# Kernel optimization log

Measured on AMD Instinct MI355X. Metric: run time of the kernel, lower is better.

Reference implementation:

```python
import jax, jax.numpy as jnp
import numpy as np

B, T, I, H, O = 256, 512, 64, 512, 1


def _lstm_layer(x, Wih, Whh, bih, bhh):
    # x: [B, T, in]; Wih: [4H, in]; Whh: [4H, H]
    # Precompute input contribution for all timesteps (big GEMM, no recurrence).
    xg = jnp.einsum('bti,gi->btg', x, Wih) + bih + bhh  # [B, T, 4H]
    h0 = jnp.zeros((x.shape[0], Whh.shape[1]), x.dtype)
    c0 = jnp.zeros_like(h0)

    def step(carry, xt):
        h, c = carry
        gates = xt + h @ Whh.T  # [B, 4H]
        i, f, g, o = jnp.split(gates, 4, axis=-1)  # PyTorch gate order i,f,g,o
        i = jax.nn.sigmoid(i)
        f = jax.nn.sigmoid(f)
        g = jnp.tanh(g)
        o = jax.nn.sigmoid(o)
        c = f * c + i * g
        h = o * jnp.tanh(c)
        return (h, c), h

    _, hs = jax.lax.scan(step, (h0, c0), jnp.swapaxes(xg, 0, 1))  # [T, B, H]
    return jnp.swapaxes(hs, 0, 1)  # [B, T, H]


def setup_inputs() -> dict:
    key = jax.random.key(0)
    ks = jax.random.split(key, 12)
    s = 1.0 / np.sqrt(H)
    u = lambda k, shp: jax.random.uniform(k, shp, jnp.float32, -s, s)
    return {
        'x': jax.random.normal(ks[0], (B, T, I), jnp.float32),
        'Wih0': u(ks[1], (4 * H, I)),
        'Whh0': u(ks[2], (4 * H, H)),
        'bih0': u(ks[3], (4 * H,)),
        'bhh0': u(ks[4], (4 * H,)),
        'Wih1': u(ks[5], (4 * H, H)),
        'Whh1': u(ks[6], (4 * H, H)),
        'bih1': u(ks[7], (4 * H,)),
        'bhh1': u(ks[8], (4 * H,)),
        'Wfc': u(ks[9], (O, H)),
        'bfc': u(ks[10], (O,)),
    }


def reference(x, Wih0, Whh0, bih0, bhh0, Wih1, Whh1, bih1, bhh1, Wfc, bfc):
    h1 = _lstm_layer(x, Wih0, Whh0, bih0, bhh0)   # [B, T, H]
    h2 = _lstm_layer(h1, Wih1, Whh1, bih1, bhh1)  # [B, T, H]
    return h2[:, -1] @ Wfc.T + bfc  # [B, O]
```

## Files before the change

kernel.cpp:

```cpp
#include <hip/hip_runtime.h>

typedef unsigned short u16;
typedef unsigned long long u64;
typedef short bf16x8 __attribute__((ext_vector_type(8)));
typedef float f32x4 __attribute__((ext_vector_type(4)));

#define B_ 256
#define T_ 512
#define I_ 64
#define H_ 512
#define RING 32

#define OFF_F0    0u
#define OFF_F1    32768u
#define OFF_F2    65536u
#define OFF_F3    98304u
#define OFF_B0    131072u
#define OFF_B1    139264u
#define OFF_WIH0  147456u
#define OFF_WHH0  409600u
#define OFF_WIH1  2506752u
#define OFF_WHH1  4603904u
#define OFF_HX0   6701056u
#define OFF_HX1   7225344u
#define OFF_H1R   7749632u
#define WS_NEEDED 16138240u

#define AQ __ATOMIC_RELAXED
#define SC __HIP_MEMORY_SCOPE_AGENT

static __device__ __forceinline__ u16 f2b(float f) {
  union { float f; unsigned u; } v; v.f = f;
  unsigned r = (v.u + 0x7FFFu + ((v.u >> 16) & 1u)) >> 16;
  return (u16)r;
}
static __device__ __forceinline__ float sigm(float x) { return 1.f / (1.f + __expf(-x)); }
static __device__ __forceinline__ float tanh_(float x) { return 1.f - 2.f / (__expf(2.f * x) + 1.f); }

__global__ void prep_kernel(const float* __restrict__ Wih0, const float* __restrict__ Whh0,
                            const float* __restrict__ bih0, const float* __restrict__ bhh0,
                            const float* __restrict__ Wih1, const float* __restrict__ Whh1,
                            const float* __restrict__ bih1, const float* __restrict__ bhh1,
                            const float* __restrict__ bfc, float* __restrict__ out,
                            char* __restrict__ ws) {
  unsigned* flags = (unsigned*)(ws + OFF_F0);
  float* b0 = (float*)(ws + OFF_B0);
  float* b1 = (float*)(ws + OFF_B1);
  u16* wih0b = (u16*)(ws + OFF_WIH0);
  u16* whh0b = (u16*)(ws + OFF_WHH0);
  u16* wih1b = (u16*)(ws + OFF_WIH1);
  u16* whh1b = (u16*)(ws + OFF_WHH1);

  long long i = (long long)blockIdx.x * 256 + threadIdx.x;
  if (i < 32768) { __hip_atomic_store(&flags[i], 0u, AQ, SC); return; }
  i -= 32768;
  if (i < 256) { out[i] = bfc[0]; return; }
  i -= 256;
  if (i < 2048) { b0[i] = bih0[i] + bhh0[i]; return; }
  i -= 2048;
  if (i < 2048) { b1[i] = bih1[i] + bhh1[i]; return; }
  i -= 2048;
  if (i < 131072) { wih0b[i] = f2b(Wih0[i]); return; }
  i -= 131072;
  if (i < 1048576) { whh0b[i] = f2b(Whh0[i]); return; }
  i -= 1048576;
  if (i < 1048576) { wih1b[i] = f2b(Wih1[i]); return; }
  i -= 1048576;
  if (i < 1048576) { whh1b[i] = f2b(Whh1[i]); return; }
}

template <bool IS_L0>
__device__ __forceinline__ void lstm_body(
    int bx,
    const float* __restrict__ x,
    const u16* __restrict__ Wib,
    const u16* __restrict__ Whb,
    const float* __restrict__ bias,
    unsigned* __restrict__ hx32,
    u16* __restrict__ h1ring,
    const float* __restrict__ Wfc, float* __restrict__ out,
    unsigned* __restrict__ fR,
    unsigned* __restrict__ fP,
    unsigned* __restrict__ fC,
    float* __restrict__ Gp_s, u16* __restrict__ Ax_s)
{
  const int tid = threadIdx.x;
  const int wv = tid >> 6;
  const int lane = tid & 63;
  const int quad = lane >> 4;
  const int l15 = lane & 15;
  const int jn = bx & 31;
  const int ib = bx >> 5;

  bf16x8 Bh[4][4];
#pragma unroll
  for (int r = 0; r < 4; ++r)
#pragma unroll
    for (int nt = 0; nt < 4; ++nt)
      Bh[r][nt] = *(const bf16x8*)&Whb[(size_t)(nt * 512 + jn * 16 + l15) * 512 +
                                       (wv * 4 + r) * 32 + quad * 8];
  bf16x8 Bx[4][4];
  bf16x8 Bx0[4];
  if constexpr (IS_L0) {
    if (wv < 2) {
#pragma unroll
      for (int nt = 0; nt < 4; ++nt)
        Bx0[nt] = *(const bf16x8*)&Wib[(size_t)(nt * 512 + jn * 16 + l15) * 64 +
                                       wv * 32 + quad * 8];
    }
  } else {
#pragma unroll
    for (int r = 0; r < 4; ++r)
#pragma unroll
      for (int nt = 0; nt < 4; ++nt)
        Bx[r][nt] = *(const bf16x8*)&Wib[(size_t)(nt * 512 + jn * 16 + l15) * 512 +
                                         (wv * 4 + r) * 32 + quad * 8];
  }

  const int erow = tid >> 3;
  const int ecp = tid & 7;
  float bias2[4][2];
#pragma unroll
  for (int g = 0; g < 4; ++g) {
    bias2[g][0] = bias[g * 512 + jn * 16 + 2 * ecp];
    bias2[g][1] = bias[g * 512 + jn * 16 + 2 * ecp + 1];
  }
  float cst2[2] = {0.f, 0.f};
  const f32x4 zf = {0.f, 0.f, 0.f, 0.f};
  const unsigned lineoff = ((unsigned)ib * 32 + jn) * 32;

  const int bg = ib * 32 + erow;
  const int hg = jn * 16 + 2 * ecp;
  const unsigned stoff = (unsigned)(((hg >> 3) * 256 + bg) * 4 + (ecp & 3));

  for (int t = 0; t < T_; ++t) {
    if constexpr (IS_L0) {
      int row = tid >> 3, cc = (tid & 7) * 8;
      const float* xp = x + ((size_t)(ib * 32 + row) * T_ + t) * 64 + cc;
      float4 a = *(const float4*)xp;
      float4 b = *(const float4*)(xp + 4);
      uint4 v;
      v.x = (unsigned)f2b(a.x) | ((unsigned)f2b(a.y) << 16);
      v.y = (unsigned)f2b(a.z) | ((unsigned)f2b(a.w) << 16);
      v.z = (unsigned)f2b(b.x) | ((unsigned)f2b(b.y) << 16);
      v.w = (unsigned)f2b(b.z) | ((unsigned)f2b(b.w) << 16);
      *(uint4*)&Ax_s[row * 72 + cc] = v;
      __syncthreads();
    }

    f32x4 acc[2][4];
#pragma unroll
    for (int mt = 0; mt < 2; ++mt)
#pragma unroll
      for (int nt = 0; nt < 4; ++nt) acc[mt][nt] = zf;

    if constexpr (IS_L0) {
      if (wv < 2) {
        int kk = wv * 32 + quad * 8;
        bf16x8 a0 = *(const bf16x8*)&Ax_s[l15 * 72 + kk];
        bf16x8 a1 = *(const bf16x8*)&Ax_s[(16 + l15) * 72 + kk];
#pragma unroll
        for (int nt = 0; nt < 4; ++nt) {
          acc[0][nt] = __builtin_amdgcn_mfma_f32_16x16x32_bf16(a0, Bx0[nt], acc[0][nt], 0, 0, 0);
          acc[1][nt] = __builtin_amdgcn_mfma_f32_16x16x32_bf16(a1, Bx0[nt], acc[1][nt], 0, 0, 0);
        }
      }
      if (t && wv == 0) {
        unsigned tgtR = (unsigned)t;
        unsigned tgtC = (t >= RING) ? (unsigned)(t - RING + 1) : 0u;
        for (;;) {
          unsigned vv, tg;
          if (lane < 32) { vv = __hip_atomic_load(&fR[lineoff + lane], AQ, SC); tg = tgtR; }
          else           { vv = __hip_atomic_load(&fC[lineoff + lane - 32], AQ, SC); tg = tgtC; }
          if (!__any(vv < tg)) break;
        }
      }
      __syncthreads();
    } else {
      if (wv == 0) {
        unsigned tgtP = (unsigned)(t + 1);
        unsigned tgtR = (unsigned)t;
        for (;;) {
          unsigned vv, tg;
          if (lane < 32) { vv = __hip_atomic_load(&fP[lineoff + lane], AQ, SC); tg = tgtP; }
          else           { vv = __hip_atomic_load(&fR[lineoff + lane - 32], AQ, SC); tg = tgtR; }
          if (!__any(vv < tg)) break;
        }
      }
      __syncthreads();
      const u64* hq1 = (const u64*)h1ring + (size_t)(t & (RING - 1)) * (B_ * H_ / 4);
#pragma unroll
      for (int r = 0; r < 4; ++r) {
        int ks = wv * 4 + r;
        bf16x8 af[2];
#pragma unroll
        for (int mt = 0; mt < 2; ++mt) {
          const u64* p = hq1 + (size_t)((ks * 4 + quad) * 256 + ib * 32 + mt * 16 + l15) * 2;
          union { u64 q[2]; bf16x8 v; } u;
          u.q[0] = __hip_atomic_load(p, AQ, SC);
          u.q[1] = __hip_atomic_load(p + 1, AQ, SC);
          af[mt] = u.v;
        }
#pragma unroll
        for (int nt = 0; nt < 4; ++nt) {
          acc[0][nt] = __builtin_amdgcn_mfma_f32_16x16x32_bf16(af[0], Bx[r][nt], acc[0][nt], 0, 0, 0);
          acc[1][nt] = __builtin_amdgcn_mfma_f32_16x16x32_bf16(af[1], Bx[r][nt], acc[1][nt], 0, 0, 0);
        }
      }
    }

    if (t) {
      const u64* hq = (const u64*)hx32 + (size_t)(t & 1) * (B_ * H_ / 4);
      bf16x8 af[4][2];
#pragma unroll
      for (int r = 0; r < 4; ++r) {
        int ks = wv * 4 + r;
#pragma unroll
        for (int mt = 0; mt < 2; ++mt) {
          const u64* p = hq + (size_t)((ks * 4 + quad) * 256 + ib * 32 + mt * 16 + l15) * 2;
          union { u64 q[2]; bf16x8 v; } u;
          u.q[0] = __hip_atomic_load(p, AQ, SC);
          u.q[1] = __hip_atomic_load(p + 1, AQ, SC);
          af[r][mt] = u.v;
        }
      }
#pragma unroll
      for (int r = 0; r < 4; ++r)
#pragma unroll
        for (int mt = 0; mt < 2; ++mt)
#pragma unroll
          for (int nt = 0; nt < 4; ++nt)
            acc[mt][nt] = __builtin_amdgcn_mfma_f32_16x16x32_bf16(af[r][mt], Bh[r][nt],
                                                                  acc[mt][nt], 0, 0, 0);
    }

#pragma unroll
    for (int mt = 0; mt < 2; ++mt)
#pragma unroll
      for (int nt = 0; nt < 4; ++nt)
#pragma unroll
        for (int rr = 0; rr < 4; ++rr)
          Gp_s[(wv * 32 + mt * 16 + quad * 4 + rr) * 68 + nt * 16 + l15] = acc[mt][nt][rr];
    __syncthreads();

    {
      float pre[4][2];
#pragma unroll
      for (int g = 0; g < 4; ++g) {
        int c = g * 16 + 2 * ecp;
        float s0 = bias2[g][0], s1 = bias2[g][1];
#pragma unroll
        for (int w = 0; w < 4; ++w) {
          s0 += Gp_s[(w * 32 + erow) * 68 + c];
          s1 += Gp_s[(w * 32 + erow) * 68 + c + 1];
        }
        pre[g][0] = s0; pre[g][1] = s1;
      }
      float hv[2];
#pragma unroll
      for (int j = 0; j < 2; ++j) {
        float iv = sigm(pre[0][j]);
        float fv = sigm(pre[1][j]);
        float gv = tanh_(pre[2][j]);
        float ov = sigm(pre[3][j]);
        float cn = fv * cst2[j] + iv * gv;
        cst2[j] = cn;
        hv[j] = ov * tanh_(cn);
      }
      unsigned pack = (unsigned)f2b(hv[0]) | ((unsigned)f2b(hv[1]) << 16);
      __hip_atomic_store(&hx32[(size_t)((t + 1) & 1) * (B_ * H_ / 2) + stoff], pack, AQ, SC);
      if constexpr (IS_L0) {
        unsigned* ring32 = (unsigned*)h1ring;
        __hip_atomic_store(&ring32[(size_t)(t & (RING - 1)) * (B_ * H_ / 2) + stoff],
                           pack, AQ, SC);
      } else if (t == T_ - 1) {
        float part = hv[0] * Wfc[hg] + hv[1] * Wfc[hg + 1];
        part += __shfl_down(part, 4, 8);
        part += __shfl_down(part, 2, 8);
        part += __shfl_down(part, 1, 8);
        if (ecp == 0) atomicAdd(&out[bg], part);
      }
    }

    if constexpr (IS_L0) {
      __syncthreads();
      if (wv == 0) {
        unsigned val = (unsigned)(t + 1);
        if (lane < 32) {
          if (t + 1 < T_)
            __hip_atomic_store(&fR[((unsigned)ib * 32 + lane) * 32 + jn], val, AQ, SC);
        } else {
          __hip_atomic_store(&fP[((unsigned)ib * 32 + (lane - 32)) * 32 + jn], val, AQ, SC);
        }
      }
    } else {
      if (t + 1 < T_) {
        __syncthreads();
        if (wv == 0) {
          unsigned val = (unsigned)(t + 1);
          if (lane < 32)
            __hip_atomic_store(&fR[((unsigned)ib * 32 + lane) * 32 + jn], val, AQ, SC);
          else
            __hip_atomic_store(&fC[((unsigned)ib * 32 + (lane - 32)) * 32 + jn], val, AQ, SC);
        }
      }
    }
  }
}

__global__ __launch_bounds__(256, 2) void lstm_fused(
    const float* __restrict__ x,
    const u16* __restrict__ wih0, const u16* __restrict__ whh0, const float* __restrict__ b0,
    const u16* __restrict__ wih1, const u16* __restrict__ whh1, const float* __restrict__ b1,
    unsigned* __restrict__ hx0, unsigned* __restrict__ hx1, u16* __restrict__ h1ring,
    const float* __restrict__ Wfc, float* __restrict__ out,
    unsigned* __restrict__ f0, unsigned* __restrict__ f1, unsigned* __restrict__ f2,
    unsigned* __restrict__ f3)
{
  __shared__ __align__(16) float Gp_s[4 * 32 * 68];
  __shared__ __align__(16) u16 Ax_s[32 * 72];
  if (blockIdx.x < 256)
    lstm_body<true>(blockIdx.x, x, wih0, whh0, b0, hx0, h1ring,
                    (const float*)nullptr, (float*)nullptr, f0, f1, f3, Gp_s, Ax_s);
  else
    lstm_body<false>(blockIdx.x - 256, (const float*)nullptr, wih1, whh1, b1, hx1, h1ring,
                     Wfc, out, f2, f1, f3, Gp_s, Ax_s);
}

extern "C" void kernel_launch(void* const* d_in, const int* in_sizes, int n_in,
                              void* d_out, int out_size, void* d_ws, size_t ws_size,
                              hipStream_t stream) {
  if (ws_size < (size_t)WS_NEEDED) return;

  const float* x    = (const float*)d_in[0];
  const float* Wih0 = (const float*)d_in[1];
  const float* Whh0 = (const float*)d_in[2];
  const float* bih0 = (const float*)d_in[3];
  const float* bhh0 = (const float*)d_in[4];
  const float* Wih1 = (const float*)d_in[5];
  const float* Whh1 = (const float*)d_in[6];
  const float* bih1 = (const float*)d_in[7];
  const float* bhh1 = (const float*)d_in[8];
  const float* Wfc  = (const float*)d_in[9];
  const float* bfc  = (const float*)d_in[10];

  char* ws = (char*)d_ws;
  unsigned* f0   = (unsigned*)(ws + OFF_F0);
  unsigned* f1   = (unsigned*)(ws + OFF_F1);
  unsigned* f2   = (unsigned*)(ws + OFF_F2);
  unsigned* f3   = (unsigned*)(ws + OFF_F3);
  float* b0      = (float*)(ws + OFF_B0);
  float* b1      = (float*)(ws + OFF_B1);
  u16* wih0b     = (u16*)(ws + OFF_WIH0);
  u16* whh0b     = (u16*)(ws + OFF_WHH0);
  u16* wih1b     = (u16*)(ws + OFF_WIH1);
  u16* whh1b     = (u16*)(ws + OFF_WHH1);
  unsigned* hx0  = (unsigned*)(ws + OFF_HX0);
  unsigned* hx1  = (unsigned*)(ws + OFF_HX1);
  u16* h1ring    = (u16*)(ws + OFF_H1R);
  float* out     = (float*)d_out;

  prep_kernel<<<12948, 256, 0, stream>>>(Wih0, Whh0, bih0, bhh0, Wih1, Whh1, bih1, bhh1,
                                         bfc, out, ws);

  lstm_fused<<<512, 256, 0, stream>>>(x, wih0b, whh0b, b0, wih1b, whh1b, b1,
                                      hx0, hx1, h1ring, Wfc, out, f0, f1, f2, f3);
}
```

Before: 2.930 ms.

## Switch to per-wave progress flags and double-buffered LDS to drop block barriers

Replaces the per-block flag matrices with per-wave progress counters, one per (batch group, column block, wave), that each wave publishes after draining its stores. All waves now poll directly, which removes the trailing __syncthreads and the pre-poll barrier. Gate partials are double-buffered in LDS so the next step can begin without an extra barrier. Layer 0 reads its recurrent state straight from the h1 ring instead of a separate hx buffer, and loads x directly into registers rather than staging it through LDS. The costs are more polling traffic, with every wave spinning on flags, and a larger LDS footprint, which may limit the 2-blocks-per-CU target.

```diff
diff --git a/kernel.cpp b/kernel.cpp
--- a/kernel.cpp
+++ b/kernel.cpp
@@ -12,19 +12,17 @@
 #define RING 32
 
 #define OFF_F0    0u
-#define OFF_F1    32768u
-#define OFF_F2    65536u
-#define OFF_F3    98304u
-#define OFF_B0    131072u
-#define OFF_B1    139264u
-#define OFF_WIH0  147456u
-#define OFF_WHH0  409600u
-#define OFF_WIH1  2506752u
-#define OFF_WHH1  4603904u
-#define OFF_HX0   6701056u
-#define OFF_HX1   7225344u
-#define OFF_H1R   7749632u
-#define WS_NEEDED 16138240u
+#define OFF_F2    4096u
+#define OFF_F3    8192u
+#define OFF_B0    12288u
+#define OFF_B1    20480u
+#define OFF_WIH0  28672u
+#define OFF_WHH0  290816u
+#define OFF_WIH1  2387968u
+#define OFF_WHH1  4485120u
+#define OFF_HX1   6582272u
+#define OFF_H1R   7106560u
+#define WS_NEEDED 15495168u
 
 #define AQ __ATOMIC_RELAXED
 #define SC __HIP_MEMORY_SCOPE_AGENT
@@ -52,8 +50,8 @@
   u16* whh1b = (u16*)(ws + OFF_WHH1);
 
   long long i = (long long)blockIdx.x * 256 + threadIdx.x;
-  if (i < 32768) { __hip_atomic_store(&flags[i], 0u, AQ, SC); return; }
-  i -= 32768;
+  if (i < 3072) { __hip_atomic_store(&flags[i], 0u, AQ, SC); return; }
+  i -= 3072;
   if (i < 256) { out[i] = bfc[0]; return; }
   i -= 256;
   if (i < 2048) { b0[i] = bih0[i] + bhh0[i]; return; }
@@ -79,10 +77,10 @@
     unsigned* __restrict__ hx32,
     u16* __restrict__ h1ring,
     const float* __restrict__ Wfc, float* __restrict__ out,
-    unsigned* __restrict__ fR,
-    unsigned* __restrict__ fP,
-    unsigned* __restrict__ fC,
-    float* __restrict__ Gp_s, u16* __restrict__ Ax_s)
+    unsigned* __restrict__ Fown,
+    unsigned* __restrict__ Fin,
+    unsigned* __restrict__ Fcr,
+    float* __restrict__ Gp_s)
 {
   const int tid = threadIdx.x;
   const int wv = tid >> 6;
@@ -127,67 +125,73 @@
   }
   float cst2[2] = {0.f, 0.f};
   const f32x4 zf = {0.f, 0.f, 0.f, 0.f};
-  const unsigned lineoff = ((unsigned)ib * 32 + jn) * 32;
 
   const int bg = ib * 32 + erow;
   const int hg = jn * 16 + 2 * ecp;
   const unsigned stoff = (unsigned)(((hg >> 3) * 256 + bg) * 4 + (ecp & 3));
 
+  const int fown_idx = ib * 128 + jn * 4 + wv;
+  const unsigned* __restrict__ pollOwn = Fown + ib * 128 + wv * 32;
+  const unsigned* __restrict__ pollIn  = IS_L0 ? (const unsigned*)nullptr
+                                               : Fin + ib * 128 + wv * 32;
+  const unsigned* __restrict__ pollCr  = Fcr + ib * 128 + (jn >> 3);
+
   for (int t = 0; t < T_; ++t) {
+    f32x4 acc[2][4];
+#pragma unroll
+    for (int mt = 0; mt < 2; ++mt)
+#pragma unroll
+      for (int nt = 0; nt < 4; ++nt) acc[mt][nt] = zf;
+
     if constexpr (IS_L0) {
-      int row = tid >> 3, cc = (tid & 7) * 8;
-      const float* xp = x + ((size_t)(ib * 32 + row) * T_ + t) * 64 + cc;
-      float4 a = *(const float4*)xp;
-      float4 b = *(const float4*)(xp + 4);
-      uint4 v;
-      v.x = (unsigned)f2b(a.x) | ((unsigned)f2b(a.y) << 16);
-      v.y = (unsigned)f2b(a.z) | ((unsigned)f2b(a.w) << 16);
-      v.z = (unsigned)f2b(b.x) | ((unsigned)f2b(b.y) << 16);
-      v.w = (unsigned)f2b(b.z) | ((unsigned)f2b(b.w) << 16);
-      *(uint4*)&Ax_s[row * 72 + cc] = v;
-      __syncthreads();
-    }
-
-    f32x4 acc[2][4];
-#pragma unroll
-    for (int mt = 0; mt < 2; ++mt)
-#pragma unroll
-      for (int nt = 0; nt < 4; ++nt) acc[mt][nt] = zf;
-
-    if constexpr (IS_L0) {
+      float4 xa, xb, xc, xd;
       if (wv < 2) {
-        int kk = wv * 32 + quad * 8;
-        bf16x8 a0 = *(const bf16x8*)&Ax_s[l15 * 72 + kk];
-        bf16x8 a1 = *(const bf16x8*)&Ax_s[(16 + l15) * 72 + kk];
-#pragma unroll
-        for (int nt = 0; nt < 4; ++nt) {
-          acc[0][nt] = __builtin_amdgcn_mfma_f32_16x16x32_bf16(a0, Bx0[nt], acc[0][nt], 0, 0, 0);
-          acc[1][nt] = __builtin_amdgcn_mfma_f32_16x16x32_bf16(a1, Bx0[nt], acc[1][nt], 0, 0, 0);
-        }
-      }
-      if (t && wv == 0) {
-        unsigned tgtR = (unsigned)t;
-        unsigned tgtC = (t >= RING) ? (unsigned)(t - RING + 1) : 0u;
+        const float* xp = x + ((size_t)(ib * 32 + l15) * T_ + t) * 64 + wv * 32 + quad * 8;
+        const float* xq = xp + (size_t)16 * T_ * 64;
+        xa = *(const float4*)xp;  xb = *(const float4*)(xp + 4);
+        xc = *(const float4*)xq;  xd = *(const float4*)(xq + 4);
+      }
+      if (t) {
+        const unsigned tgtF = (unsigned)t;
+        const bool cchk = (wv == 0) && (t >= RING);
+        const unsigned tgtC = cchk ? (unsigned)(t - (RING - 1)) : 0u;
         for (;;) {
           unsigned vv, tg;
-          if (lane < 32) { vv = __hip_atomic_load(&fR[lineoff + lane], AQ, SC); tg = tgtR; }
-          else           { vv = __hip_atomic_load(&fC[lineoff + lane - 32], AQ, SC); tg = tgtC; }
+          if (cchk && lane >= 32) {
+            vv = __hip_atomic_load(&pollCr[(lane - 32) * 4], AQ, SC); tg = tgtC;
+          } else {
+            vv = __hip_atomic_load(&pollOwn[lane & 31], AQ, SC); tg = tgtF;
+          }
           if (!__any(vv < tg)) break;
         }
       }
-      __syncthreads();
+      if (wv < 2) {
+        union { unsigned u[4]; bf16x8 v; } P0, P1;
+        P0.u[0] = (unsigned)f2b(xa.x) | ((unsigned)f2b(xa.y) << 16);
+        P0.u[1] = (unsigned)f2b(xa.z) | ((unsigned)f2b(xa.w) << 16);
+        P0.u[2] = (unsigned)f2b(xb.x) | ((unsigned)f2b(xb.y) << 16);
+        P0.u[3] = (unsigned)f2b(xb.z) | ((unsigned)f2b(xb.w) << 16);
+        P1.u[0] = (unsigned)f2b(xc.x) | ((unsigned)f2b(xc.y) << 16);
+        P1.u[1] = (unsigned)f2b(xc.z) | ((unsigned)f2b(xc.w) << 16);
+        P1.u[2] = (unsigned)f2b(xd.x) | ((unsigned)f2b(xd.y) << 16);
+        P1.u[3] = (unsigned)f2b(xd.z) | ((unsigned)f2b(xd.w) << 16);
+#pragma unroll
+        for (int nt = 0; nt < 4; ++nt) {
+          acc[0][nt] = __builtin_amdgcn_mfma_f32_16x16x32_bf16(P0.v, Bx0[nt], acc[0][nt], 0, 0, 0);
+          acc[1][nt] = __builtin_amdgcn_mfma_f32_16x16x32_bf16(P1.v, Bx0[nt], acc[1][nt], 0, 0, 0);
+        }
+      }
     } else {
-      if (wv == 0) {
-        unsigned tgtP = (unsigned)(t + 1);
-        unsigned tgtR = (unsigned)t;
+      {
+        const unsigned tgtI = (unsigned)(t + 1);
+        const unsigned tgtR = (unsigned)t;
         for (;;) {
           unsigned vv, tg;
-          if (lane < 32) { vv = __hip_atomic_load(&fP[lineoff + lane], AQ, SC); tg = tgtP; }
-          else           { vv = __hip_atomic_load(&fR[lineoff + lane - 32], AQ, SC); tg = tgtR; }
+          if (lane < 32) { vv = __hip_atomic_load(&pollIn[lane], AQ, SC); tg = tgtI; }
+          else           { vv = __hip_atomic_load(&pollOwn[lane - 32], AQ, SC); tg = tgtR; }
           if (!__any(vv < tg)) break;
         }
       }
-      __syncthreads();
       const u64* hq1 = (const u64*)h1ring + (size_t)(t & (RING - 1)) * (B_ * H_ / 4);
 #pragma unroll
       for (int r = 0; r < 4; ++r) {
@@ -210,7 +214,11 @@
     }
 
     if (t) {
-      const u64* hq = (const u64*)hx32 + (size_t)(t & 1) * (B_ * H_ / 4);
+      const u64* hq;
+      if constexpr (IS_L0)
+        hq = (const u64*)h1ring + (size_t)((t - 1) & (RING - 1)) * (B_ * H_ / 4);
+      else
+        hq = (const u64*)hx32 + (size_t)(t & 1) * (B_ * H_ / 4);
       bf16x8 af[4][2];
 #pragma unroll
       for (int r = 0; r < 4; ++r) {
@@ -234,13 +242,14 @@
                                                                   acc[mt][nt], 0, 0, 0);
     }
 
+    float* __restrict__ Gp = Gp_s + (t & 1) * (4 * 32 * 68);
 #pragma unroll
     for (int mt = 0; mt < 2; ++mt)
 #pragma unroll
       for (int nt = 0; nt < 4; ++nt)
 #pragma unroll
         for (int rr = 0; rr < 4; ++rr)
-          Gp_s[(wv * 32 + mt * 16 + quad * 4 + rr) * 68 + nt * 16 + l15] = acc[mt][nt][rr];
+          Gp[(wv * 32 + mt * 16 + quad * 4 + rr) * 68 + nt * 16 + l15] = acc[mt][nt][rr];
     __syncthreads();
 
     {
@@ -251,8 +260,8 @@
         float s0 = bias2[g][0], s1 = bias2[g][1];
 #pragma unroll
         for (int w = 0; w < 4; ++w) {
-          s0 += Gp_s[(w * 32 + erow) * 68 + c];
-          s1 += Gp_s[(w * 32 + erow) * 68 + c + 1];
+          s0 += Gp[(w * 32 + erow) * 68 + c];
+          s1 += Gp[(w * 32 + erow) * 68 + c + 1];
         }
         pre[g][0] = s0; pre[g][1] = s1;
       }
@@ -268,42 +277,27 @@
         hv[j] = ov * tanh_(cn);
       }
       unsigned pack = (unsigned)f2b(hv[0]) | ((unsigned)f2b(hv[1]) << 16);
-      __hip_atomic_store(&hx32[(size_t)((t + 1) & 1) * (B_ * H_ / 2) + stoff], pack, AQ, SC);
       if constexpr (IS_L0) {
         unsigned* ring32 = (unsigned*)h1ring;
         __hip_atomic_store(&ring32[(size_t)(t & (RING - 1)) * (B_ * H_ / 2) + stoff],
                            pack, AQ, SC);
-      } else if (t == T_ - 1) {
-        float part = hv[0] * Wfc[hg] + hv[1] * Wfc[hg + 1];
-        part += __shfl_down(part, 4, 8);
-        part += __shfl_down(part, 2, 8);
-        part += __shfl_down(part, 1, 8);
-        if (ecp == 0) atomicAdd(&out[bg], part);
-      }
-    }
-
-    if constexpr (IS_L0) {
-      __syncthreads();
-      if (wv == 0) {
-        unsigned val = (unsigned)(t + 1);
-        if (lane < 32) {
-          if (t + 1 < T_)
-            __hip_atomic_store(&fR[((unsigned)ib * 32 + lane) * 32 + jn], val, AQ, SC);
-        } else {
-          __hip_atomic_store(&fP[((unsigned)ib * 32 + (lane - 32)) * 32 + jn], val, AQ, SC);
-        }
-      }
-    } else {
-      if (t + 1 < T_) {
-        __syncthreads();
-        if (wv == 0) {
-          unsigned val = (unsigned)(t + 1);
-          if (lane < 32)
-            __hip_atomic_store(&fR[((unsigned)ib * 32 + lane) * 32 + jn], val, AQ, SC);
-          else
-            __hip_atomic_store(&fC[((unsigned)ib * 32 + (lane - 32)) * 32 + jn], val, AQ, SC);
-        }
-      }
+      } else {
+        __hip_atomic_store(&hx32[(size_t)((t + 1) & 1) * (B_ * H_ / 2) + stoff], pack, AQ, SC);
+        if (t == T_ - 1) {
+          float part = hv[0] * Wfc[hg] + hv[1] * Wfc[hg + 1];
+          part += __shfl_down(part, 4, 8);
+          part += __shfl_down(part, 2, 8);
+          part += __shfl_down(part, 1, 8);
+          if (ecp == 0) atomicAdd(&out[bg], part);
+        }
+      }
+    }
+
+    asm volatile("s_waitcnt vmcnt(0)" ::: "memory");
+    if (lane == 0) {
+      __hip_atomic_store(&Fown[fown_idx], (unsigned)(t + 1), AQ, SC);
+      if constexpr (!IS_L0)
+        __hip_atomic_store(&Fcr[fown_idx], (unsigned)(t + 1), AQ, SC);
     }
   }
 }
@@ -312,19 +306,17 @@
     const float* __restrict__ x,
     const u16* __restrict__ wih0, const u16* __restrict__ whh0, const float* __restrict__ b0,
     const u16* __restrict__ wih1, const u16* __restrict__ whh1, const float* __restrict__ b1,
-    unsigned* __restrict__ hx0, unsigned* __restrict__ hx1, u16* __restrict__ h1ring,
+    unsigned* __restrict__ hx1, u16* __restrict__ h1ring,
     const float* __restrict__ Wfc, float* __restrict__ out,
-    unsigned* __restrict__ f0, unsigned* __restrict__ f1, unsigned* __restrict__ f2,
-    unsigned* __restrict__ f3)
+    unsigned* __restrict__ f0, unsigned* __restrict__ f2, unsigned* __restrict__ f3)
 {
-  __shared__ __align__(16) float Gp_s[4 * 32 * 68];
-  __shared__ __align__(16) u16 Ax_s[32 * 72];
+  __shared__ __align__(16) float Gp_s[2 * 4 * 32 * 68];
   if (blockIdx.x < 256)
-    lstm_body<true>(blockIdx.x, x, wih0, whh0, b0, hx0, h1ring,
-                    (const float*)nullptr, (float*)nullptr, f0, f1, f3, Gp_s, Ax_s);
+    lstm_body<true>(blockIdx.x, x, wih0, whh0, b0, (unsigned*)nullptr, h1ring,
+                    (const float*)nullptr, (float*)nullptr, f0, (unsigned*)nullptr, f3, Gp_s);
   else
     lstm_body<false>(blockIdx.x - 256, (const float*)nullptr, wih1, whh1, b1, hx1, h1ring,
-                     Wfc, out, f2, f1, f3, Gp_s, Ax_s);
+                     Wfc, out, f2, f0, f3, Gp_s);
 }
 
 extern "C" void kernel_launch(void* const* d_in, const int* in_sizes, int n_in,
@@ -346,7 +338,6 @@
 
   char* ws = (char*)d_ws;
   unsigned* f0   = (unsigned*)(ws + OFF_F0);
-  unsigned* f1   = (unsigned*)(ws + OFF_F1);
   unsigned* f2   = (unsigned*)(ws + OFF_F2);
   unsigned* f3   = (unsigned*)(ws + OFF_F3);
   float* b0      = (float*)(ws + OFF_B0);
@@ -355,14 +346,13 @@
   u16* whh0b     = (u16*)(ws + OFF_WHH0);
   u16* wih1b     = (u16*)(ws + OFF_WIH1);
   u16* whh1b     = (u16*)(ws + OFF_WHH1);
-  unsigned* hx0  = (unsigned*)(ws + OFF_HX0);
   unsigned* hx1  = (unsigned*)(ws + OFF_HX1);
   u16* h1ring    = (u16*)(ws + OFF_H1R);
   float* out     = (float*)d_out;
 
-  prep_kernel<<<12948, 256, 0, stream>>>(Wih0, Whh0, bih0, bhh0, Wih1, Whh1, bih1, bhh1,
+  prep_kernel<<<12829, 256, 0, stream>>>(Wih0, Whh0, bih0, bhh0, Wih1, Whh1, bih1, bhh1,
                                          bfc, out, ws);
 
   lstm_fused<<<512, 256, 0, stream>>>(x, wih0b, whh0b, b0, wih1b, whh1b, b1,
-                                      hx0, hx1, h1ring, Wfc, out, f0, f1, f2, f3);
-}
+                                      hx1, h1ring, Wfc, out, f0, f2, f3);
+}
```

Result: slower. 4.752 ms (+62.2%).

## Read layer-0 recurrent state from ring buffer and load x directly into MFMA fragments

Applied to the files above, without the earlier changes.

Layer 0 no longer writes a separate double-buffered hidden-state array. It reads h_{t-1} from the ring slot that layer 1 already consumes, which removes one global store per element per step. The x input is loaded and converted to bf16 straight into MFMA operand registers, dropping the LDS staging buffer and one __syncthreads per step. The trade-off is that the ring must not be overwritten before layer 0 reads it, which relies on the existing consumer flag, and the x loads are now less coalesced.

```diff
diff --git a/kernel.cpp b/kernel.cpp
--- a/kernel.cpp
+++ b/kernel.cpp
@@ -21,10 +21,9 @@
 #define OFF_WHH0  409600u
 #define OFF_WIH1  2506752u
 #define OFF_WHH1  4603904u
-#define OFF_HX0   6701056u
-#define OFF_HX1   7225344u
-#define OFF_H1R   7749632u
-#define WS_NEEDED 16138240u
+#define OFF_HX1   6701056u
+#define OFF_H1R   7225344u
+#define WS_NEEDED 15613952u
 
 #define AQ __ATOMIC_RELAXED
 #define SC __HIP_MEMORY_SCOPE_AGENT
@@ -82,7 +81,7 @@
     unsigned* __restrict__ fR,
     unsigned* __restrict__ fP,
     unsigned* __restrict__ fC,
-    float* __restrict__ Gp_s, u16* __restrict__ Ax_s)
+    float* __restrict__ Gp_s)
 {
   const int tid = threadIdx.x;
   const int wv = tid >> 6;
@@ -134,20 +133,6 @@
   const unsigned stoff = (unsigned)(((hg >> 3) * 256 + bg) * 4 + (ecp & 3));
 
   for (int t = 0; t < T_; ++t) {
-    if constexpr (IS_L0) {
-      int row = tid >> 3, cc = (tid & 7) * 8;
-      const float* xp = x + ((size_t)(ib * 32 + row) * T_ + t) * 64 + cc;
-      float4 a = *(const float4*)xp;
-      float4 b = *(const float4*)(xp + 4);
-      uint4 v;
-      v.x = (unsigned)f2b(a.x) | ((unsigned)f2b(a.y) << 16);
-      v.y = (unsigned)f2b(a.z) | ((unsigned)f2b(a.w) << 16);
-      v.z = (unsigned)f2b(b.x) | ((unsigned)f2b(b.y) << 16);
-      v.w = (unsigned)f2b(b.z) | ((unsigned)f2b(b.w) << 16);
-      *(uint4*)&Ax_s[row * 72 + cc] = v;
-      __syncthreads();
-    }
-
     f32x4 acc[2][4];
 #pragma unroll
     for (int mt = 0; mt < 2; ++mt)
@@ -156,13 +141,25 @@
 
     if constexpr (IS_L0) {
       if (wv < 2) {
-        int kk = wv * 32 + quad * 8;
-        bf16x8 a0 = *(const bf16x8*)&Ax_s[l15 * 72 + kk];
-        bf16x8 a1 = *(const bf16x8*)&Ax_s[(16 + l15) * 72 + kk];
+        const float* xp = x + ((size_t)(ib * 32 + l15) * T_ + t) * 64 + wv * 32 + quad * 8;
+        const float* xq = xp + (size_t)16 * T_ * 64;
+        float4 xa = *(const float4*)xp;
+        float4 xb = *(const float4*)(xp + 4);
+        float4 xc = *(const float4*)xq;
+        float4 xd = *(const float4*)(xq + 4);
+        union { unsigned u[4]; bf16x8 v; } P0, P1;
+        P0.u[0] = (unsigned)f2b(xa.x) | ((unsigned)f2b(xa.y) << 16);
+        P0.u[1] = (unsigned)f2b(xa.z) | ((unsigned)f2b(xa.w) << 16);
+        P0.u[2] = (unsigned)f2b(xb.x) | ((unsigned)f2b(xb.y) << 16);
+        P0.u[3] = (unsigned)f2b(xb.z) | ((unsigned)f2b(xb.w) << 16);
+        P1.u[0] = (unsigned)f2b(xc.x) | ((unsigned)f2b(xc.y) << 16);
+        P1.u[1] = (unsigned)f2b(xc.z) | ((unsigned)f2b(xc.w) << 16);
+        P1.u[2] = (unsigned)f2b(xd.x) | ((unsigned)f2b(xd.y) << 16);
+        P1.u[3] = (unsigned)f2b(xd.z) | ((unsigned)f2b(xd.w) << 16);
 #pragma unroll
         for (int nt = 0; nt < 4; ++nt) {
-          acc[0][nt] = __builtin_amdgcn_mfma_f32_16x16x32_bf16(a0, Bx0[nt], acc[0][nt], 0, 0, 0);
-          acc[1][nt] = __builtin_amdgcn_mfma_f32_16x16x32_bf16(a1, Bx0[nt], acc[1][nt], 0, 0, 0);
+          acc[0][nt] = __builtin_amdgcn_mfma_f32_16x16x32_bf16(P0.v, Bx0[nt], acc[0][nt], 0, 0, 0);
+          acc[1][nt] = __builtin_amdgcn_mfma_f32_16x16x32_bf16(P1.v, Bx0[nt], acc[1][nt], 0, 0, 0);
         }
       }
       if (t && wv == 0) {
@@ -210,7 +207,11 @@
     }
 
     if (t) {
-      const u64* hq = (const u64*)hx32 + (size_t)(t & 1) * (B_ * H_ / 4);
+      const u64* hq;
+      if constexpr (IS_L0)
+        hq = (const u64*)h1ring + (size_t)((t - 1) & (RING - 1)) * (B_ * H_ / 4);
+      else
+        hq = (const u64*)hx32 + (size_t)(t & 1) * (B_ * H_ / 4);
       bf16x8 af[4][2];
 #pragma unroll
       for (int r = 0; r < 4; ++r) {
@@ -268,36 +269,34 @@
         hv[j] = ov * tanh_(cn);
       }
       unsigned pack = (unsigned)f2b(hv[0]) | ((unsigned)f2b(hv[1]) << 16);
-      __hip_atomic_store(&hx32[(size_t)((t + 1) & 1) * (B_ * H_ / 2) + stoff], pack, AQ, SC);
       if constexpr (IS_L0) {
         unsigned* ring32 = (unsigned*)h1ring;
         __hip_atomic_store(&ring32[(size_t)(t & (RING - 1)) * (B_ * H_ / 2) + stoff],
                            pack, AQ, SC);
-      } else if (t == T_ - 1) {
-        float part = hv[0] * Wfc[hg] + hv[1] * Wfc[hg + 1];
-        part += __shfl_down(part, 4, 8);
-        part += __shfl_down(part, 2, 8);
-        part += __shfl_down(part, 1, 8);
-        if (ecp == 0) atomicAdd(&out[bg], part);
-      }
-    }
-
-    if constexpr (IS_L0) {
-      __syncthreads();
-      if (wv == 0) {
-        unsigned val = (unsigned)(t + 1);
+      } else {
+        __hip_atomic_store(&hx32[(size_t)((t + 1) & 1) * (B_ * H_ / 2) + stoff], pack, AQ, SC);
+        if (t == T_ - 1) {
+          float part = hv[0] * Wfc[hg] + hv[1] * Wfc[hg + 1];
+          part += __shfl_down(part, 4, 8);
+          part += __shfl_down(part, 2, 8);
+          part += __shfl_down(part, 1, 8);
+          if (ecp == 0) atomicAdd(&out[bg], part);
+        }
+      }
+    }
+
+    __syncthreads();
+    if (wv == 0) {
+      unsigned val = (unsigned)(t + 1);
+      if constexpr (IS_L0) {
         if (lane < 32) {
           if (t + 1 < T_)
             __hip_atomic_store(&fR[((unsigned)ib * 32 + lane) * 32 + jn], val, AQ, SC);
         } else {
           __hip_atomic_store(&fP[((unsigned)ib * 32 + (lane - 32)) * 32 + jn], val, AQ, SC);
         }
-      }
-    } else {
-      if (t + 1 < T_) {
-        __syncthreads();
-        if (wv == 0) {
-          unsigned val = (unsigned)(t + 1);
+      } else {
+        if (t + 1 < T_) {
           if (lane < 32)
             __hip_atomic_store(&fR[((unsigned)ib * 32 + lane) * 32 + jn], val, AQ, SC);
           else
@@ -312,19 +311,18 @@
     const float* __restrict__ x,
     const u16* __restrict__ wih0, const u16* __restrict__ whh0, const float* __restrict__ b0,
     const u16* __restrict__ wih1, const u16* __restrict__ whh1, const float* __restrict__ b1,
-    unsigned* __restrict__ hx0, unsigned* __restrict__ hx1, u16* __restrict__ h1ring,
+    unsigned* __restrict__ hx1, u16* __restrict__ h1ring,
     const float* __restrict__ Wfc, float* __restrict__ out,
     unsigned* __restrict__ f0, unsigned* __restrict__ f1, unsigned* __restrict__ f2,
     unsigned* __restrict__ f3)
 {
   __shared__ __align__(16) float Gp_s[4 * 32 * 68];
-  __shared__ __align__(16) u16 Ax_s[32 * 72];
   if (blockIdx.x < 256)
-    lstm_body<true>(blockIdx.x, x, wih0, whh0, b0, hx0, h1ring,
-                    (const float*)nullptr, (float*)nullptr, f0, f1, f3, Gp_s, Ax_s);
+    lstm_body<true>(blockIdx.x, x, wih0, whh0, b0, (unsigned*)nullptr, h1ring,
+                    (const float*)nullptr, (float*)nullptr, f0, f1, f3, Gp_s);
   else
     lstm_body<false>(blockIdx.x - 256, (const float*)nullptr, wih1, whh1, b1, hx1, h1ring,
-                     Wfc, out, f2, f1, f3, Gp_s, Ax_s);
+                     Wfc, out, f2, f1, f3, Gp_s);
 }
 
 extern "C" void kernel_launch(void* const* d_in, const int* in_sizes, int n_in,
@@ -355,7 +353,6 @@
   u16* whh0b     = (u16*)(ws + OFF_WHH0);
   u16* wih1b     = (u16*)(ws + OFF_WIH1);
   u16* whh1b     = (u16*)(ws + OFF_WHH1);
-  unsigned* hx0  = (unsigned*)(ws + OFF_HX0);
   unsigned* hx1  = (unsigned*)(ws + OFF_HX1);
   u16* h1ring    = (u16*)(ws + OFF_H1R);
   float* out     = (float*)d_out;
@@ -364,5 +361,5 @@
                                          bfc, out, ws);
 
   lstm_fused<<<512, 256, 0, stream>>>(x, wih0b, whh0b, b0, wih1b, whh1b, b1,
-                                      hx0, hx1, h1ring, Wfc, out, f0, f1, f2, f3);
-}
+                                      hx1, h1ring, Wfc, out, f0, f1, f2, f3);
+}
```

New measurement: 2.848 ms. -2.8%, faster.
